# Performance work log

Hardware: AMD Instinct MI355X
Metric: run time of the kernel (lower is better)

## Reference

```python
import jax, jax.numpy as jnp
import numpy as np
from jax import lax


def setup_inputs() -> dict:
    key = jax.random.key(0)
    ks = jax.random.split(key, 6)
    B, C, H, W = 8, 128, 64, 64   # C = 2*channel, channel (per-branch) c = 64
    c = C // 2
    return {
        "x_up": jax.random.normal(ks[0], (B, C, H, W), dtype=jnp.float32),
        "x_skip": jax.random.normal(ks[1], (B, C, H, W), dtype=jnp.float32),
        # nn.Linear(c, 2c): weight [out,in], bias [out]
        "kv1_w": jax.random.normal(ks[2], (2 * c, c), dtype=jnp.float32) * 0.05,
        "kv1_b": jnp.zeros((2 * c,), dtype=jnp.float32),
        "kv2_w": jax.random.normal(ks[3], (2 * c, c), dtype=jnp.float32) * 0.05,
        "kv2_b": jnp.zeros((2 * c,), dtype=jnp.float32),
        # Conv2d(2c, 2c, 3, stride 1, pad 1, bias=False), OIHW
        "conv_w": jax.random.normal(ks[4], (C, C, 3, 3), dtype=jnp.float32) * 0.05,
        # BatchNorm2d(2c) in inference form (running stats)
        "bn_gamma": jax.random.normal(ks[5], (C,), dtype=jnp.float32) * 0.1 + 1.0,
        "bn_beta": jnp.zeros((C,), dtype=jnp.float32),
        "bn_mean": jnp.zeros((C,), dtype=jnp.float32),
        "bn_var": jnp.ones((C,), dtype=jnp.float32),
    }


def reference(x_up, x_skip, kv1_w, kv1_b, kv2_w, kv2_b, conv_w,
              bn_gamma, bn_beta, bn_mean, bn_var):
    b, C, h, w = x_up.shape
    c = C // 2
    hw = h * w
    up1, up2 = x_up[:, :c], x_up[:, c:]
    sk1, sk2 = x_skip[:, :c], x_skip[:, c:]

    # ---- spatial attention branch (softmax over last axis, hw x hw) ----
    shortcut1 = up1 + sk1
    u1 = up1.reshape(b, c, hw).transpose(0, 2, 1)   # (b, hw, c)
    s1 = sk1.reshape(b, c, hw).transpose(0, 2, 1)   # (b, hw, c)
    kv = s1 @ kv1_w.T + kv1_b                        # (b, hw, 2c)
    k1, v1 = kv[..., :c], kv[..., c:]
    attn = jax.nn.softmax(jnp.einsum('bnc,bmc->bnm', u1, k1), axis=-1)  # (b, hw, hw)
    sout = jnp.einsum('bnm,bmc->bnc', attn, v1)      # (b, hw, c)
    sout = sout.transpose(0, 2, 1).reshape(b, c, h, w) + shortcut1

    # ---- channel attention branch (softmax over dim=1 of the c x c map) ----
    shortcut2 = up2 + sk2
    u2 = up2.reshape(b, c, hw).transpose(0, 2, 1)    # (b, hw, c)
    s2 = sk2.reshape(b, c, hw).transpose(0, 2, 1)
    kv = s2 @ kv2_w.T + kv2_b                        # (b, hw, 2c)
    k2, v2 = kv[..., :c], kv[..., c:]
    A = jax.nn.softmax(jnp.einsum('bnc,bnd->bcd', u2, k2), axis=1)  # (b, c, c)
    cout = jnp.einsum('bnc,bcd->bnd', v2, A)          # (b, hw, c)
    cout = cout.transpose(0, 2, 1).reshape(b, c, h, w) + shortcut2

    # ---- conv + BN (inference) + ReLU ----
    x = jnp.concatenate([sout, cout], axis=1)         # (b, 2c, h, w)
    y = lax.conv_general_dilated(x, conv_w, (1, 1), 'SAME',
                                 dimension_numbers=('NCHW', 'OIHW', 'NCHW'))
    inv = jax.lax.rsqrt(bn_var + 1e-5)
    y = (y - bn_mean[None, :, None, None]) * (inv * bn_gamma)[None, :, None, None] \
        + bn_beta[None, :, None, None]
    return jax.nn.relu(y)
```

## Files before the change

kernel.cpp:

```cpp
#include <hip/hip_runtime.h>
#include <math.h>

#define HW 4096

typedef __attribute__((ext_vector_type(8))) short bh8;
typedef __attribute__((ext_vector_type(4))) float f32x4;
typedef __attribute__((ext_vector_type(2))) unsigned int u32x2;
typedef unsigned int u32;
typedef unsigned short u16;

__device__ __forceinline__ u16 f2bf(float f) {
  union { float f; u32 u; } v; v.f = f;
  u32 u = v.u;
  return (u16)((u + 0x7FFFu + ((u >> 16) & 1u)) >> 16);
}
__device__ __forceinline__ float bf2f(u16 h) {
  union { u32 u; float f; } v; v.u = ((u32)h) << 16;
  return v.f;
}
__device__ __forceinline__ float ubits2f(u32 u) {
  union { u32 u; float f; } v; v.u = u;
  return v.f;
}
__device__ __forceinline__ u32 cvt_pk_bf16(float lo, float hi) {
  u32 r;
  asm("v_cvt_pk_bf16_f32 %0, %1, %2" : "=v"(r) : "v"(lo), "v"(hi));
  return r;
}
__device__ __forceinline__ float fexp2(float x) {
  float r;
  asm("v_exp_f32 %0, %1" : "=v"(r) : "v"(x));
  return r;
}

__global__ __launch_bounds__(256) void kv_proj(
    const float* __restrict__ xs,
    const float* __restrict__ w1, const float* __restrict__ b1,
    const float* __restrict__ w2, const float* __restrict__ b2,
    u32* __restrict__ Knm, u16* __restrict__ Vcm,
    u16* __restrict__ K2t, u16* __restrict__ V2t,
    const float* __restrict__ cw, const float* __restrict__ gamma,
    const float* __restrict__ beta, const float* __restrict__ mean,
    const float* __restrict__ var, u16* __restrict__ Wg,
    float* __restrict__ shb) {
  __shared__ __align__(16) u16 XsH[64][72];
  __shared__ __align__(16) u16 XsL[64][72];
  __shared__ u32 LtK[64][33];
  const int b = blockIdx.y, n0 = blockIdx.x * 64;
  const int t = threadIdx.x;
  const int wq = t >> 6, lane = t & 63, lq = lane & 15, quad = lane >> 4;
  const float* xsb = xs + (size_t)b * 128 * HW;

  {
    int gid = (blockIdx.y * 64 + blockIdx.x) * 256 + t;
    for (int i = gid; i < 147456; i += 131072) {
      int tap = i >> 14, oc = (i >> 7) & 127, ic = i & 127;
      float sc = gamma[oc] * rsqrtf(var[oc] + 1e-5f);
      Wg[i] = f2bf(cw[((size_t)(oc * 128 + ic)) * 9 + tap] * sc);
    }
    if (gid < 128) {
      float sc = gamma[gid] * rsqrtf(var[gid] + 1e-5f);
      shb[gid] = beta[gid] - mean[gid] * sc;
    }
  }

  for (int br = 0; br < 2; ++br) {
    const float* W = br ? w2 : w1;
    const float* bias = br ? b2 : b1;
    const float* src = xsb + (br ? 64 * HW : 0);

    bh8 wh[2][2], wl[2][2];
#pragma unroll
    for (int jt = 0; jt < 2; ++jt)
#pragma unroll
      for (int s = 0; s < 2; ++s) {
        const float* wr = W + (size_t)(wq * 32 + jt * 16 + lq) * 64 + s * 32 + quad * 8;
        float4 a0 = *(const float4*)wr;
        float4 a1 = *(const float4*)(wr + 4);
        float f[8] = {a0.x, a0.y, a0.z, a0.w, a1.x, a1.y, a1.z, a1.w};
        union { u32 u[4]; bh8 v; } H, L;
#pragma unroll
        for (int p = 0; p < 4; ++p) {
          u32 hp = cvt_pk_bf16(f[2 * p], f[2 * p + 1]);
          float h0 = ubits2f(hp << 16);
          float h1 = ubits2f(hp & 0xFFFF0000u);
          H.u[p] = hp;
          L.u[p] = cvt_pk_bf16(f[2 * p] - h0, f[2 * p + 1] - h1);
        }
        wh[jt][s] = H.v;
        wl[jt][s] = L.v;
      }

    if (br) __syncthreads();
    {
      const int n = t & 63, cg = t >> 6;
#pragma unroll
      for (int s8 = 0; s8 < 8; ++s8) {
        int ch0 = s8 * 8 + cg * 2;
        float f0 = src[(size_t)ch0 * HW + n0 + n];
        float f1 = src[(size_t)(ch0 + 1) * HW + n0 + n];
        u32 hp = cvt_pk_bf16(f0, f1);
        float h0 = ubits2f(hp << 16);
        float h1 = ubits2f(hp & 0xFFFF0000u);
        u32 lp = cvt_pk_bf16(f0 - h0, f1 - h1);
        *(u32*)&XsH[n][ch0] = hp;
        *(u32*)&XsL[n][ch0] = lp;
      }
    }
    __syncthreads();

    f32x4 acc[2][4];
#pragma unroll
    for (int nt = 0; nt < 4; ++nt) {
      const int xr = nt * 16 + lq;
      bh8 xh0 = *(const bh8*)&XsH[xr][quad * 8];
      bh8 xh1 = *(const bh8*)&XsH[xr][32 + quad * 8];
      bh8 xl0 = *(const bh8*)&XsL[xr][quad * 8];
      bh8 xl1 = *(const bh8*)&XsL[xr][32 + quad * 8];
#pragma unroll
      for (int jt = 0; jt < 2; ++jt) {
        f32x4 a = (f32x4)(0.f);
        a = __builtin_amdgcn_mfma_f32_16x16x32_bf16(wh[jt][0], xh0, a, 0, 0, 0);
        a = __builtin_amdgcn_mfma_f32_16x16x32_bf16(wh[jt][1], xh1, a, 0, 0, 0);
        a = __builtin_amdgcn_mfma_f32_16x16x32_bf16(wh[jt][0], xl0, a, 0, 0, 0);
        a = __builtin_amdgcn_mfma_f32_16x16x32_bf16(wh[jt][1], xl1, a, 0, 0, 0);
        a = __builtin_amdgcn_mfma_f32_16x16x32_bf16(wl[jt][0], xh0, a, 0, 0, 0);
        a = __builtin_amdgcn_mfma_f32_16x16x32_bf16(wl[jt][1], xh1, a, 0, 0, 0);
        acc[jt][nt] = a;
      }
    }

    if (br == 0) {
      if (wq < 2) {
#pragma unroll
        for (int jt = 0; jt < 2; ++jt) {
          float4 bv = *(const float4*)&bias[wq * 32 + jt * 16 + quad * 4];
#pragma unroll
          for (int nt = 0; nt < 4; ++nt) {
            f32x4 a = acc[jt][nt];
            LtK[nt * 16 + lq][wq * 16 + jt * 8 + quad * 2] =
                cvt_pk_bf16(a[0] + bv.x, a[1] + bv.y);
            LtK[nt * 16 + lq][wq * 16 + jt * 8 + quad * 2 + 1] =
                cvt_pk_bf16(a[2] + bv.z, a[3] + bv.w);
          }
        }
      } else {
#pragma unroll
        for (int jt = 0; jt < 2; ++jt) {
          float4 bv = *(const float4*)&bias[wq * 32 + jt * 16 + quad * 4];
          float bvv[4] = {bv.x, bv.y, bv.z, bv.w};
#pragma unroll
          for (int nt = 0; nt < 4; ++nt)
#pragma unroll
            for (int r = 0; r < 4; ++r) {
              int ch = (wq - 2) * 32 + jt * 16 + quad * 4 + r;
              Vcm[((size_t)b * 64 + ch) * HW + n0 + nt * 16 + lq] =
                  f2bf(acc[jt][nt][r] + bvv[r]);
            }
        }
      }
      __syncthreads();
#pragma unroll
      for (int p = 0; p < 8; ++p) {
        int idx = p * 256 + t;
        int n = idx >> 5, cc = idx & 31;
        Knm[((size_t)b * HW + n0 + n) * 32 + cc] = LtK[n][cc];
      }
    } else {
      u16* base = (wq < 2) ? (K2t + (size_t)b * 64 * HW) : (V2t + (size_t)b * 64 * HW);
      const int chb = (wq & 1) * 32;
#pragma unroll
      for (int jt = 0; jt < 2; ++jt) {
        float4 bv = *(const float4*)&bias[wq * 32 + jt * 16 + quad * 4];
        float bvv[4] = {bv.x, bv.y, bv.z, bv.w};
#pragma unroll
        for (int nt = 0; nt < 4; ++nt)
#pragma unroll
          for (int r = 0; r < 4; ++r) {
            int ch = chb + jt * 16 + quad * 4 + r;
            base[(size_t)ch * HW + n0 + nt * 16 + lq] =
                f2bf(acc[jt][nt][r] + bvv[r]);
          }
      }
    }
  }
}

__device__ __forceinline__ void attn_step(
    const bh8* kf, const bh8* vf, const bh8 (&qb)[4][2], const bh8 ones,
    f32x4 (&O)[4][4], f32x4 (&Osum)[4]) {
  f32x4 S[2][4];
  __builtin_amdgcn_s_setprio(1);
#pragma unroll
  for (int mt = 0; mt < 2; ++mt)
#pragma unroll
    for (int nt = 0; nt < 4; ++nt) {
      f32x4 a = (f32x4)(0.f);
      a = __builtin_amdgcn_mfma_f32_16x16x32_bf16(kf[mt * 2 + 0], qb[nt][0], a, 0, 0, 0);
      a = __builtin_amdgcn_mfma_f32_16x16x32_bf16(kf[mt * 2 + 1], qb[nt][1], a, 0, 0, 0);
      S[mt][nt] = a;
    }
  __builtin_amdgcn_s_setprio(0);
#pragma unroll
  for (int nt = 0; nt < 4; ++nt) {
    const float c = 17.312340f;
    float e00 = fexp2(S[0][nt][0] - c), e01 = fexp2(S[0][nt][1] - c);
    float e02 = fexp2(S[0][nt][2] - c), e03 = fexp2(S[0][nt][3] - c);
    float e10 = fexp2(S[1][nt][0] - c), e11 = fexp2(S[1][nt][1] - c);
    float e12 = fexp2(S[1][nt][2] - c), e13 = fexp2(S[1][nt][3] - c);
    u32 A = cvt_pk_bf16(e00, e01);
    u32 B = cvt_pk_bf16(e02, e03);
    u32 C = cvt_pk_bf16(e10, e11);
    u32 D = cvt_pk_bf16(e12, e13);
    u32x2 rac = __builtin_amdgcn_permlane32_swap(A, C, 0, 0);
    u32x2 rbd = __builtin_amdgcn_permlane32_swap(B, D, 0, 0);
    u32x2 r02 = __builtin_amdgcn_permlane16_swap(rac.x, rac.y, 0, 0);
    u32x2 r13 = __builtin_amdgcn_permlane16_swap(rbd.x, rbd.y, 0, 0);
    union { u32 u[4]; bh8 v; } pb;
    pb.u[0] = r02.x;
    pb.u[1] = r13.x;
    pb.u[2] = r02.y;
    pb.u[3] = r13.y;
    __builtin_amdgcn_s_setprio(1);
#pragma unroll
    for (int ct = 0; ct < 4; ++ct)
      O[ct][nt] = __builtin_amdgcn_mfma_f32_16x16x32_bf16(vf[ct], pb.v, O[ct][nt], 0, 0, 0);
    Osum[nt] = __builtin_amdgcn_mfma_f32_16x16x32_bf16(ones, pb.v, Osum[nt], 0, 0, 0);
    __builtin_amdgcn_s_setprio(0);
  }
}

#define LOADKV(KB, KF, VF)                                            \
  do {                                                                \
    const int n0_ = (KB) * 128;                                       \
    const u16* kr_ = Kb + (size_t)(n0_ + wb + lq) * 64 + quad * 8;    \
    KF[0] = *(const bh8*)(kr_);                                       \
    KF[1] = *(const bh8*)(kr_ + 32);                                  \
    KF[2] = *(const bh8*)(kr_ + 1024);                                \
    KF[3] = *(const bh8*)(kr_ + 1056);                                \
    const u16* vr_ = Vb + (size_t)lq * HW + n0_ + wb + quad * 8;      \
    VF[0] = *(const bh8*)(vr_);                                       \
    VF[1] = *(const bh8*)(vr_ + 16 * HW);                             \
    VF[2] = *(const bh8*)(vr_ + 32 * HW);                             \
    VF[3] = *(const bh8*)(vr_ + 48 * HW);                             \
  } while (0)

__global__ __launch_bounds__(256, 2) void attn_gram(
    const float* __restrict__ xu, const float* __restrict__ xs,
    const u16* __restrict__ Knm, const u16* __restrict__ Vcm,
    u16* __restrict__ xcat,
    const u16* __restrict__ K2t, float* __restrict__ Mp) {
  __shared__ __align__(16) u16 SMEM[18432];
  const int b = blockIdx.y;
  const int t = threadIdx.x;

  if (blockIdx.x >= 64) {
    float* Us = (float*)SMEM;
    float* Ksm = Us + 64 * 65;
    const int n0 = (blockIdx.x - 64) * 128;
    const int c = t & 63, dg = t >> 6;
    const float* ub = xu + ((size_t)b * 128 + 64) * HW;
    const u16* kb2 = K2t + (size_t)b * 64 * HW;
    float acc[16];
#pragma unroll
    for (int i = 0; i < 16; ++i) acc[i] = 0.f;
    for (int s = 0; s < 2; ++s) {
      int nn = n0 + s * 64;
      __syncthreads();
      for (int r = 0; r < 16; ++r) {
        int row = r * 4 + dg;
        Us[row * 65 + c] = ub[(size_t)row * HW + nn + c];
        Ksm[row * 65 + c] = bf2f(kb2[(size_t)row * HW + nn + c]);
      }
      __syncthreads();
      for (int n = 0; n < 64; ++n) {
        float u = Us[c * 65 + n];
#pragma unroll
        for (int i = 0; i < 16; ++i)
          acc[i] = fmaf(Ksm[(dg * 16 + i) * 65 + n], u, acc[i]);
      }
    }
    float* dst = Mp + ((size_t)(blockIdx.x - 64) * 8 + b) * 4096 + c * 64 + dg * 16;
#pragma unroll
    for (int i = 0; i < 16; ++i) dst[i] = acc[i];
    return;
  }

  const int q0 = blockIdx.x * 64;
  const int wq = t >> 6, lane = t & 63, lq = lane & 15, quad = lane >> 4;
  const int wb = wq * 32;
  const float* xub = xu + (size_t)b * 128 * HW;
  const float* xsb = xs + (size_t)b * 128 * HW;
  const u16* Kb = Knm + (size_t)b * HW * 64;
  const u16* Vb = Vcm + (size_t)b * 64 * HW;

  bh8 qb[4][2];
#pragma unroll
  for (int nt = 0; nt < 4; ++nt)
#pragma unroll
    for (int s = 0; s < 2; ++s)
#pragma unroll
      for (int j = 0; j < 8; ++j) {
        int ch = s * 32 + quad * 8 + j;
        qb[nt][s][j] =
            (short)f2bf(xub[(size_t)ch * HW + q0 + nt * 16 + lq] * 1.44269504f);
      }
  bh8 ones;
#pragma unroll
  for (int j = 0; j < 8; ++j) ones[j] = (short)0x3F80;

  f32x4 O[4][4];
#pragma unroll
  for (int ct = 0; ct < 4; ++ct)
#pragma unroll
    for (int nt = 0; nt < 4; ++nt) O[ct][nt] = (f32x4)(0.f);
  f32x4 Osum[4];
#pragma unroll
  for (int nt = 0; nt < 4; ++nt) Osum[nt] = (f32x4)(0.f);

  bh8 kfa[4], vfa[4], kfb[4], vfb[4];
  LOADKV(0, kfa, vfa);
  for (int kb = 0; kb < 32; kb += 2) {
    LOADKV(kb + 1, kfb, vfb);
    attn_step(kfa, vfa, qb, ones, O, Osum);
    if (kb + 2 < 32) LOADKV(kb + 2, kfa, vfa);
    attn_step(kfb, vfb, qb, ones, O, Osum);
  }

  float* Posc = (float*)SMEM;
  float* Lred = (float*)(SMEM + 17408);
  if (quad == 0) {
#pragma unroll
    for (int nt = 0; nt < 4; ++nt) Lred[(wq * 4 + nt) * 16 + lq] = Osum[nt][0];
  }

  const int q = t & 63, cg = t >> 6;
#pragma unroll
  for (int rh = 0; rh < 2; ++rh) {
    if (rh) __syncthreads();
#pragma unroll
    for (int c2 = 0; c2 < 2; ++c2)
#pragma unroll
      for (int nt = 0; nt < 4; ++nt)
#pragma unroll
        for (int r = 0; r < 4; ++r)
          Posc[(wq * 32 + c2 * 16 + quad * 4 + r) * 68 + nt * 16 + lq] =
              O[rh * 2 + c2][nt][r];
    __syncthreads();
    float li = 0.f;
#pragma unroll
    for (int w2 = 0; w2 < 4; ++w2) li += Lred[w2 * 64 + q];
    float inv = 1.f / li;
    u16 h[8];
#pragma unroll
    for (int i = 0; i < 8; ++i) {
      int chl = cg * 8 + i;
      float s = 0.f;
#pragma unroll
      for (int w2 = 0; w2 < 4; ++w2) s += Posc[(w2 * 32 + chl) * 68 + q];
      int ch = rh * 32 + chl;
      size_t g = (size_t)ch * HW + q0 + q;
      h[i] = f2bf(s * inv + xub[g] + xsb[g]);
    }
    u32 pk[4];
#pragma unroll
    for (int j = 0; j < 4; ++j) pk[j] = (u32)h[2 * j] | ((u32)h[2 * j + 1] << 16);
    u16* ob = xcat + ((size_t)b * HW + q0 + q) * 128 + rh * 32 + cg * 8;
    *(uint4*)ob = make_uint4(pk[0], pk[1], pk[2], pk[3]);
  }
}

__global__ void chan_reduce(const float* __restrict__ Mp, float* __restrict__ M) {
  int idx = blockIdx.x * 256 + threadIdx.x;
  float s = 0.f;
  for (int ch = 0; ch < 32; ++ch) s += Mp[(size_t)ch * 32768 + idx];
  M[idx] = s;
}

__global__ __launch_bounds__(256) void chan_apply(
    const u16* __restrict__ V2t, const float* __restrict__ M,
    const float* __restrict__ xu, const float* __restrict__ xs,
    u16* __restrict__ xcat) {
  __shared__ float Vsm[64][65];
  __shared__ float As[64][65];
  __shared__ float red1[4][64], red2[4][64];
  const int b = blockIdx.y, n0 = blockIdx.x * 64, t = threadIdx.x;
  const int lane = t & 63, dg = t >> 6;
  const u16* Vb = V2t + (size_t)b * 64 * HW;
  for (int s = 0; s < 16; ++s) {
    int c = s * 4 + dg;
    Vsm[lane][c] = bf2f(Vb[(size_t)c * HW + n0 + lane]);
  }
  for (int idx = t; idx < 4096; idx += 256) As[idx >> 6][idx & 63] = M[b * 4096 + idx];
  __syncthreads();
  float mx = -1e30f;
#pragma unroll
  for (int i = 0; i < 16; ++i) mx = fmaxf(mx, As[dg * 16 + i][lane]);
  red1[dg][lane] = mx;
  __syncthreads();
  mx = fmaxf(fmaxf(red1[0][lane], red1[1][lane]), fmaxf(red1[2][lane], red1[3][lane]));
  float se = 0.f;
#pragma unroll
  for (int i = 0; i < 16; ++i) {
    float e = __expf(As[dg * 16 + i][lane] - mx);
    As[dg * 16 + i][lane] = e;
    se += e;
  }
  red2[dg][lane] = se;
  __syncthreads();

  float acc[16];
#pragma unroll
  for (int i = 0; i < 16; ++i) acc[i] = 0.f;
  for (int c = 0; c < 64; ++c) {
    float v = Vsm[lane][c];
#pragma unroll
    for (int i = 0; i < 16; ++i) acc[i] = fmaf(v, As[c][dg * 16 + i], acc[i]);
  }
  const float* xub = xu + ((size_t)b * 128 + 64) * HW;
  const float* xsb = xs + ((size_t)b * 128 + 64) * HW;
  const int n = n0 + lane;
  u16 hv[16];
#pragma unroll
  for (int i = 0; i < 16; ++i) {
    int d = dg * 16 + i;
    float sm = red2[0][d] + red2[1][d] + red2[2][d] + red2[3][d];
    hv[i] = f2bf(acc[i] / sm + xub[(size_t)d * HW + n] + xsb[(size_t)d * HW + n]);
  }
  u32 pk[8];
#pragma unroll
  for (int j = 0; j < 8; ++j) pk[j] = (u32)hv[2 * j] | ((u32)hv[2 * j + 1] << 16);
  u16* ob = xcat + ((size_t)b * HW + n) * 128 + 64 + dg * 16;
  *(uint4*)(ob) = make_uint4(pk[0], pk[1], pk[2], pk[3]);
  *(uint4*)(ob + 8) = make_uint4(pk[4], pk[5], pk[6], pk[7]);
}

__global__ __launch_bounds__(512) void conv_mfma(
    const u16* __restrict__ X, const u16* __restrict__ Wg,
    const float* __restrict__ shb, float* __restrict__ out) {
  __shared__ __align__(16) u16 In[4 * 66 * 136];
  __shared__ __align__(16) u16 Wt[2][128 * 136];
  const int b = blockIdx.y, h0 = blockIdx.x * 2;
  const int t = threadIdx.x;
  const int wq = t >> 6, lane = t & 63, lq = lane & 15, quad = lane >> 4;
  const int nb = (wq & 1) * 64;
  const int mb = (wq >> 1) * 2;
  const u16* Xb = X + (size_t)b * HW * 128;

  if (t < 128) {
    int ih = t >> 5, iwsel = (t >> 4) & 1, ck = t & 15;
    int iw = iwsel ? 65 : 0;
    *(uint4*)&In[(ih * 66 + iw) * 136 + ck * 8] = make_uint4(0, 0, 0, 0);
  }
  for (int ih = 0; ih < 4; ++ih) {
    int h = h0 - 1 + ih;
    bool ok = (h >= 0 && h < 64);
    const u16* src = Xb + (size_t)h * 64 * 128;
#pragma unroll
    for (int p = 0; p < 2; ++p) {
      int idx = p * 512 + t;
      int row = idx >> 4, ck = idx & 15;
      uint4 d = make_uint4(0, 0, 0, 0);
      if (ok) d = *(const uint4*)(src + (size_t)row * 128 + ck * 8);
      *(uint4*)&In[(ih * 66 + 1 + row) * 136 + ck * 8] = d;
    }
  }
  {
    const u16* src = Wg;
#pragma unroll
    for (int p = 0; p < 4; ++p) {
      int idx = p * 512 + t;
      int oc = idx >> 4, ck = idx & 15;
      uint4 d = *(const uint4*)(src + oc * 128 + ck * 8);
      *(uint4*)&Wt[0][oc * 136 + ck * 8] = d;
    }
  }
  __syncthreads();

  f32x4 acc[2][4];
#pragma unroll
  for (int mt = 0; mt < 2; ++mt)
#pragma unroll
    for (int nt = 0; nt < 4; ++nt) acc[mt][nt] = (f32x4)(0.f);

  for (int tap = 0; tap < 9; ++tap) {
    const int cur = tap & 1;
    if (tap < 8) {
      const u16* src = Wg + (size_t)(tap + 1) * 128 * 128;
#pragma unroll
      for (int p = 0; p < 4; ++p) {
        int idx = p * 512 + t;
        int oc = idx >> 4, ck = idx & 15;
        uint4 d = *(const uint4*)(src + oc * 128 + ck * 8);
        *(uint4*)&Wt[cur ^ 1][oc * 136 + ck * 8] = d;
      }
    }
    const int dh = tap / 3, dw = tap - 3 * dh;
    const u16* Wc = &Wt[cur][0];
#pragma unroll
    for (int c = 0; c < 4; ++c) {
      bh8 bf[4];
#pragma unroll
      for (int nt = 0; nt < 4; ++nt)
        bf[nt] = *(const bh8*)&Wc[(nb + nt * 16 + lq) * 136 + c * 32 + quad * 8];
#pragma unroll
      for (int mt = 0; mt < 2; ++mt) {
        int s = (mb + mt) * 16 + lq;
        int ih = (s >> 6) + dh, iw = (s & 63) + dw;
        bh8 af = *(const bh8*)&In[(ih * 66 + iw) * 136 + c * 32 + quad * 8];
#pragma unroll
        for (int nt = 0; nt < 4; ++nt)
          acc[mt][nt] = __builtin_amdgcn_mfma_f32_16x16x32_bf16(af, bf[nt], acc[mt][nt], 0, 0, 0);
      }
    }
    __syncthreads();
  }

  float shv[4];
#pragma unroll
  for (int nt = 0; nt < 4; ++nt) shv[nt] = shb[nb + nt * 16 + lq];
#pragma unroll
  for (int mt = 0; mt < 2; ++mt) {
    int mtile = mb + mt;
    int h = h0 + (mtile >> 2);
    int w0 = ((mtile & 3) * 16) + quad * 4;
#pragma unroll
    for (int nt = 0; nt < 4; ++nt) {
      int oc = nb + nt * 16 + lq;
      float4 v;
      v.x = fmaxf(acc[mt][nt][0] + shv[nt], 0.f);
      v.y = fmaxf(acc[mt][nt][1] + shv[nt], 0.f);
      v.z = fmaxf(acc[mt][nt][2] + shv[nt], 0.f);
      v.w = fmaxf(acc[mt][nt][3] + shv[nt], 0.f);
      *(float4*)&out[((size_t)b * 128 + oc) * HW + h * 64 + w0] = v;
    }
  }
}

extern "C" void kernel_launch(void* const* d_in, const int* in_sizes, int n_in,
                              void* d_out, int out_size, void* d_ws, size_t ws_size,
                              hipStream_t stream) {
  const float* x_up   = (const float*)d_in[0];
  const float* x_skip = (const float*)d_in[1];
  const float* kv1_w  = (const float*)d_in[2];
  const float* kv1_b  = (const float*)d_in[3];
  const float* kv2_w  = (const float*)d_in[4];
  const float* kv2_b  = (const float*)d_in[5];
  const float* conv_w = (const float*)d_in[6];
  const float* bn_g   = (const float*)d_in[7];
  const float* bn_b   = (const float*)d_in[8];
  const float* bn_m   = (const float*)d_in[9];
  const float* bn_v   = (const float*)d_in[10];
  float* out = (float*)d_out;

  char* ws = (char*)d_ws;
  const size_t XCATB_B = (size_t)8 * HW * 128 * 2;
  const size_t KV16_B  = (size_t)8 * 64 * HW * 2;
  size_t off = 0;
  u16*   xcat = (u16*)(ws + off);   off += XCATB_B;
  u16*   K2t  = (u16*)(ws + off);   off += KV16_B;
  u16*   V2t  = (u16*)(ws + off);   off += KV16_B;
  u32*   Knm  = (u32*)(ws + off);   off += KV16_B;
  u16*   Vcm  = (u16*)(ws + off);   off += KV16_B;
  float* Mp   = (float*)(ws + off); off += (size_t)32 * 8 * 4096 * 4;
  float* M    = (float*)(ws + off); off += (size_t)8 * 4096 * 4;
  u16*   Wg   = (u16*)(ws + off);   off += (size_t)9 * 128 * 128 * 2;
  float* shb  = (float*)(ws + off); off += 512;

  kv_proj<<<dim3(64, 8), 256, 0, stream>>>(x_skip, kv1_w, kv1_b, kv2_w, kv2_b,
                                           Knm, Vcm, K2t, V2t,
                                           conv_w, bn_g, bn_b, bn_m, bn_v, Wg, shb);
  attn_gram<<<dim3(96, 8), 256, 0, stream>>>(x_up, x_skip, (const u16*)Knm, Vcm,
                                             xcat, K2t, Mp);
  chan_reduce<<<128, 256, 0, stream>>>(Mp, M);
  chan_apply<<<dim3(64, 8), 256, 0, stream>>>(V2t, M, x_up, x_skip, xcat);
  conv_mfma<<<dim3(32, 8), 512, 0, stream>>>(xcat, Wg, shb, out);
}
```

Measured before the change: 212.7 us.

## Retile conv kernel to one row by half channels per block with LDS-staged stores

The 3x3 conv kernel is re-decomposed so each 256-thread block computes one output row for half of the output channels. This quadruples the grid from 256 to 1024 blocks to improve occupancy and CU fill. Weight double-buffering is dropped in favour of a single buffer with two barriers per tap. The epilogue stages results through LDS so global float4 stores are contiguous along width. In exchange, input rows are reloaded more often (3 rows per output row instead of 4 per 2) and weight loads are no longer overlapped with compute.

```diff
diff --git a/kernel.cpp b/kernel.cpp
--- a/kernel.cpp
+++ b/kernel.cpp
@@ -435,105 +435,87 @@
   *(uint4*)(ob + 8) = make_uint4(pk[4], pk[5], pk[6], pk[7]);
 }
 
-__global__ __launch_bounds__(512) void conv_mfma(
+__global__ __launch_bounds__(256) void conv_mfma(
     const u16* __restrict__ X, const u16* __restrict__ Wg,
     const float* __restrict__ shb, float* __restrict__ out) {
-  __shared__ __align__(16) u16 In[4 * 66 * 136];
-  __shared__ __align__(16) u16 Wt[2][128 * 136];
-  const int b = blockIdx.y, h0 = blockIdx.x * 2;
+  __shared__ __align__(16) u16 In[3 * 66 * 136];
+  __shared__ __align__(16) u16 Wt[64 * 136];
+  const int b = blockIdx.y;
+  const int h = blockIdx.x >> 1;
+  const int oh = blockIdx.x & 1;
   const int t = threadIdx.x;
   const int wq = t >> 6, lane = t & 63, lq = lane & 15, quad = lane >> 4;
-  const int nb = (wq & 1) * 64;
-  const int mb = (wq >> 1) * 2;
   const u16* Xb = X + (size_t)b * HW * 128;
 
-  if (t < 128) {
-    int ih = t >> 5, iwsel = (t >> 4) & 1, ck = t & 15;
-    int iw = iwsel ? 65 : 0;
+  if (t < 96) {
+    int ih = t >> 5, rem = t & 31;
+    int iw = (rem >> 4) ? 65 : 0, ck = rem & 15;
     *(uint4*)&In[(ih * 66 + iw) * 136 + ck * 8] = make_uint4(0, 0, 0, 0);
   }
-  for (int ih = 0; ih < 4; ++ih) {
-    int h = h0 - 1 + ih;
-    bool ok = (h >= 0 && h < 64);
-    const u16* src = Xb + (size_t)h * 64 * 128;
-#pragma unroll
-    for (int p = 0; p < 2; ++p) {
-      int idx = p * 512 + t;
+  for (int ih = 0; ih < 3; ++ih) {
+    int hr = h - 1 + ih;
+    bool ok = (hr >= 0 && hr < 64);
+    const u16* src = Xb + (size_t)hr * 64 * 128;
+#pragma unroll
+    for (int p = 0; p < 4; ++p) {
+      int idx = p * 256 + t;
       int row = idx >> 4, ck = idx & 15;
       uint4 d = make_uint4(0, 0, 0, 0);
       if (ok) d = *(const uint4*)(src + (size_t)row * 128 + ck * 8);
       *(uint4*)&In[(ih * 66 + 1 + row) * 136 + ck * 8] = d;
     }
   }
-  {
-    const u16* src = Wg;
+
+  f32x4 acc[4];
+#pragma unroll
+  for (int nt = 0; nt < 4; ++nt) acc[nt] = (f32x4)(0.f);
+
+  const u16* Wsrc = Wg + (size_t)(oh * 64) * 128;
+  for (int tap = 0; tap < 9; ++tap) {
+    __syncthreads();
+    const u16* src = Wsrc + (size_t)tap * 128 * 128;
 #pragma unroll
     for (int p = 0; p < 4; ++p) {
-      int idx = p * 512 + t;
+      int idx = p * 256 + t;
       int oc = idx >> 4, ck = idx & 15;
       uint4 d = *(const uint4*)(src + oc * 128 + ck * 8);
-      *(uint4*)&Wt[0][oc * 136 + ck * 8] = d;
-    }
-  }
-  __syncthreads();
-
-  f32x4 acc[2][4];
-#pragma unroll
-  for (int mt = 0; mt < 2; ++mt)
-#pragma unroll
-    for (int nt = 0; nt < 4; ++nt) acc[mt][nt] = (f32x4)(0.f);
-
-  for (int tap = 0; tap < 9; ++tap) {
-    const int cur = tap & 1;
-    if (tap < 8) {
-      const u16* src = Wg + (size_t)(tap + 1) * 128 * 128;
-#pragma unroll
-      for (int p = 0; p < 4; ++p) {
-        int idx = p * 512 + t;
-        int oc = idx >> 4, ck = idx & 15;
-        uint4 d = *(const uint4*)(src + oc * 128 + ck * 8);
-        *(uint4*)&Wt[cur ^ 1][oc * 136 + ck * 8] = d;
-      }
-    }
+      *(uint4*)&Wt[oc * 136 + ck * 8] = d;
+    }
+    __syncthreads();
     const int dh = tap / 3, dw = tap - 3 * dh;
-    const u16* Wc = &Wt[cur][0];
 #pragma unroll
     for (int c = 0; c < 4; ++c) {
       bh8 bf[4];
 #pragma unroll
       for (int nt = 0; nt < 4; ++nt)
-        bf[nt] = *(const bh8*)&Wc[(nb + nt * 16 + lq) * 136 + c * 32 + quad * 8];
-#pragma unroll
-      for (int mt = 0; mt < 2; ++mt) {
-        int s = (mb + mt) * 16 + lq;
-        int ih = (s >> 6) + dh, iw = (s & 63) + dw;
-        bh8 af = *(const bh8*)&In[(ih * 66 + iw) * 136 + c * 32 + quad * 8];
-#pragma unroll
-        for (int nt = 0; nt < 4; ++nt)
-          acc[mt][nt] = __builtin_amdgcn_mfma_f32_16x16x32_bf16(af, bf[nt], acc[mt][nt], 0, 0, 0);
-      }
-    }
-    __syncthreads();
-  }
-
+        bf[nt] = *(const bh8*)&Wt[(nt * 16 + lq) * 136 + c * 32 + quad * 8];
+      const int s = wq * 16 + lq;
+      bh8 af = *(const bh8*)&In[(dh * 66 + s + dw) * 136 + c * 32 + quad * 8];
+#pragma unroll
+      for (int nt = 0; nt < 4; ++nt)
+        acc[nt] = __builtin_amdgcn_mfma_f32_16x16x32_bf16(af, bf[nt], acc[nt], 0, 0, 0);
+    }
+  }
+
+  __syncthreads();
+  float* T = (float*)In;
   float shv[4];
 #pragma unroll
-  for (int nt = 0; nt < 4; ++nt) shv[nt] = shb[nb + nt * 16 + lq];
-#pragma unroll
-  for (int mt = 0; mt < 2; ++mt) {
-    int mtile = mb + mt;
-    int h = h0 + (mtile >> 2);
-    int w0 = ((mtile & 3) * 16) + quad * 4;
-#pragma unroll
-    for (int nt = 0; nt < 4; ++nt) {
-      int oc = nb + nt * 16 + lq;
-      float4 v;
-      v.x = fmaxf(acc[mt][nt][0] + shv[nt], 0.f);
-      v.y = fmaxf(acc[mt][nt][1] + shv[nt], 0.f);
-      v.z = fmaxf(acc[mt][nt][2] + shv[nt], 0.f);
-      v.w = fmaxf(acc[mt][nt][3] + shv[nt], 0.f);
-      *(float4*)&out[((size_t)b * 128 + oc) * HW + h * 64 + w0] = v;
-    }
+  for (int nt = 0; nt < 4; ++nt) shv[nt] = shb[oh * 64 + nt * 16 + lq];
+#pragma unroll
+  for (int nt = 0; nt < 4; ++nt)
+#pragma unroll
+    for (int r = 0; r < 4; ++r)
+      T[(nt * 16 + lq) * 68 + wq * 16 + quad * 4 + r] =
+          fmaxf(acc[nt][r] + shv[nt], 0.f);
+  __syncthreads();
+  float* ob = out + ((size_t)b * 128 + oh * 64) * HW + h * 64;
+#pragma unroll
+  for (int p = 0; p < 4; ++p) {
+    int idx = p * 256 + t;
+    int oc = idx >> 4, w4 = (idx & 15) * 4;
+    float4 v = *(const float4*)&T[oc * 68 + w4];
+    *(float4*)&ob[(size_t)oc * HW + w4] = v;
   }
 }
 
@@ -574,5 +556,5 @@
                                              xcat, K2t, Mp);
   chan_reduce<<<128, 256, 0, stream>>>(Mp, M);
   chan_apply<<<dim3(64, 8), 256, 0, stream>>>(V2t, M, x_up, x_skip, xcat);
-  conv_mfma<<<dim3(32, 8), 512, 0, stream>>>(xcat, Wg, shb, out);
-}
+  conv_mfma<<<dim3(128, 8), 256, 0, stream>>>(xcat, Wg, shb, out);
+}
```

Measured after the change: 219.6 us. 1.03x slower.
